# Kernel tuning notes

Hardware: AMD Instinct MI355X
Metric: run time of the kernel (lower is better)

The kernel has to match this reference:

```python
import jax, jax.numpy as jnp
import numpy as np

N_NODES = 50000
N_EDGES = 1600000
D_IN = 64
D_EDGE = 64
DIMS = [128, 128, 128]  # atom_embedding_sizes
N_GRAPHS = 64


def setup_inputs() -> dict:
    key = jax.random.key(0)
    ks = jax.random.split(key, 4 + 4 * len(DIMS))
    inp = {
        "x": jax.random.normal(ks[0], (N_NODES, D_IN), dtype=jnp.float32),
        "edge_index": jax.random.randint(ks[1], (2, N_EDGES), 0, N_NODES),
        "edge_attr": jax.random.uniform(ks[2], (N_EDGES, D_EDGE), dtype=jnp.float32),
        "batch": jnp.sort(jax.random.randint(ks[3], (N_NODES,), 0, N_GRAPHS)),
    }
    in_dim = D_IN
    ki = 4
    for l, out_dim in enumerate(DIMS):
        se = 1.0 / np.sqrt(in_dim + D_EDGE)
        sr = 1.0 / np.sqrt(in_dim)
        inp[f"We{l}"] = jax.random.uniform(ks[ki + 0], (in_dim + D_EDGE, out_dim), jnp.float32, -se, se)
        inp[f"be{l}"] = jnp.zeros((out_dim,), jnp.float32)
        inp[f"Wr{l}"] = jax.random.uniform(ks[ki + 1], (in_dim, out_dim), jnp.float32, -sr, sr)
        inp[f"br{l}"] = jnp.zeros((out_dim,), jnp.float32)
        ki += 2
        in_dim = out_dim
    return inp


def reference(x, edge_index, edge_attr, batch,
              We0, be0, Wr0, br0,
              We1, be1, Wr1, br1,
              We2, be2, Wr2, br2):
    params = [(We0, be0, Wr0, br0), (We1, be1, Wr1, br1), (We2, be2, Wr2, br2)]
    src, dst = edge_index[0], edge_index[1]  # PyG convention: messages flow src -> dst
    for We, be, Wr, br in params:
        # ESAGEConv: message = Linear([x_j || edge_attr]); add-aggregate to dst;
        # root transform Linear(x_i); then ReLU (module activation).
        msg = jnp.concatenate([x[src], edge_attr], axis=-1) @ We + be  # [E, out]
        aggr = jax.ops.segment_sum(msg, dst, num_segments=N_NODES)     # [N, out]
        x = jax.nn.relu(aggr + x @ Wr + br)
    # readout_pooling='add' -> global_add_pool over graph ids
    return jax.ops.segment_sum(x, batch, num_segments=N_GRAPHS)  # [G, out]
```

## Files before the change

### kernel.cpp

```cpp
#include <hip/hip_runtime.h>
#include <hip/hip_bf16.h>
#include <cstdint>

typedef __attribute__((ext_vector_type(8))) short short8v;
typedef __attribute__((ext_vector_type(4))) short short4v;
typedef __attribute__((ext_vector_type(4))) float f32x4;

__device__ __forceinline__ float4 add4(float4 a, float4 b) {
  return make_float4(a.x + b.x, a.y + b.y, a.z + b.z, a.w + b.w);
}
__device__ __forceinline__ float bf2f(unsigned short u) {
  union { unsigned int i; float f; } v; v.i = ((unsigned int)u) << 16; return v.f;
}
__device__ __forceinline__ unsigned short f2bf(float f) {
  union { float f; unsigned int i; } v; v.f = f;
  unsigned int r = v.i + 0x7fff + ((v.i >> 16) & 1);
  return (unsigned short)(r >> 16);
}
__device__ __forceinline__ float4 shflx4(float4 a, int m) {
  return make_float4(__shfl_xor(a.x, m, 64), __shfl_xor(a.y, m, 64),
                     __shfl_xor(a.z, m, 64), __shfl_xor(a.w, m, 64));
}
__device__ __forceinline__ void acc8(float4& lo, float4& hi, short8v v) {
  lo.x += bf2f((unsigned short)v[0]); lo.y += bf2f((unsigned short)v[1]);
  lo.z += bf2f((unsigned short)v[2]); lo.w += bf2f((unsigned short)v[3]);
  hi.x += bf2f((unsigned short)v[4]); hi.y += bf2f((unsigned short)v[5]);
  hi.z += bf2f((unsigned short)v[6]); hi.w += bf2f((unsigned short)v[7]);
}


__global__ void count_deg_kernel(const int* __restrict__ dst, int* __restrict__ deg, int E) {
  int i = blockIdx.x * blockDim.x + threadIdx.x;
  if (i < E) atomicAdd(&deg[dst[i]], 1);
}

__global__ void block_sum_kernel(const int* __restrict__ deg, int* __restrict__ bsum, int N) {
  int t = threadIdx.x;
  int i = blockIdx.x * 512 + t;
  int v = (i < N) ? deg[i] : 0;
#pragma unroll
  for (int off = 32; off > 0; off >>= 1) v += __shfl_down(v, off, 64);
  __shared__ int ws[8];
  int lane = t & 63, wid = t >> 6;
  if (lane == 0) ws[wid] = v;
  __syncthreads();
  if (t == 0) {
    int s = 0;
#pragma unroll
    for (int j = 0; j < 8; ++j) s += ws[j];
    bsum[blockIdx.x] = s;
  }
}

__global__ void scan_small_kernel(const int* __restrict__ bsum, int* __restrict__ boffs, int B) {
  int t = threadIdx.x;
  int lane = t & 63, wid = t >> 6;
  int v = (t < B) ? bsum[t] : 0;
  int incl = v;
#pragma unroll
  for (int off = 1; off < 64; off <<= 1) {
    int u = __shfl_up(incl, off, 64);
    if (lane >= off) incl += u;
  }
  __shared__ int ws[2];
  if (lane == 63) ws[wid] = incl;
  __syncthreads();
  int base = (wid == 1) ? ws[0] : 0;
  if (t < B) boffs[t] = base + incl - v;
}

__global__ void ptrs_kernel(const int* __restrict__ deg, const int* __restrict__ boffs,
                            int* __restrict__ ptrs, int N) {
  int t = threadIdx.x;
  int i = blockIdx.x * 512 + t;
  int lane = t & 63, wid = t >> 6;
  int v = (i < N) ? deg[i] : 0;
  int incl = v;
#pragma unroll
  for (int off = 1; off < 64; off <<= 1) {
    int u = __shfl_up(incl, off, 64);
    if (lane >= off) incl += u;
  }
  __shared__ int ws[8];
  if (lane == 63) ws[wid] = incl;
  __syncthreads();
  if (t == 0) {
    int s = 0;
#pragma unroll
    for (int j = 0; j < 8; ++j) { int tmp = ws[j]; ws[j] = s; s += tmp; }
  }
  __syncthreads();
  if (i < N) ptrs[i + 1] = boffs[blockIdx.x] + ws[wid] + incl;
  if (i == 0 && blockIdx.x == 0) ptrs[0] = 0;
}

__global__ void fill_csr_kernel(const int* __restrict__ src, const int* __restrict__ dst,
                                const int* __restrict__ ptrs, int* __restrict__ cnt,
                                int2* __restrict__ csr, int E) {
  int i = blockIdx.x * blockDim.x + threadIdx.x;
  if (i < E) {
    int d = dst[i];
    int pos = ptrs[d] + atomicAdd(&cnt[d], 1);
    csr[pos] = make_int2(src[i], i);
  }
}


__global__ void f2bf_stream_kernel(const float* __restrict__ in, unsigned short* __restrict__ out, int n) {
  int i = (blockIdx.x * blockDim.x + threadIdx.x) * 8;
  if (i < n) {
    float4 v0 = *(const float4*)(in + i);
    float4 v1 = *(const float4*)(in + i + 4);
    short8v o;
    o[0] = (short)f2bf(v0.x); o[1] = (short)f2bf(v0.y);
    o[2] = (short)f2bf(v0.z); o[3] = (short)f2bf(v0.w);
    o[4] = (short)f2bf(v1.x); o[5] = (short)f2bf(v1.y);
    o[6] = (short)f2bf(v1.z); o[7] = (short)f2bf(v1.w);
    *(short8v*)(out + i) = o;
  }
}

__global__ void pack_all_kernel(const float* __restrict__ We0, const float* __restrict__ Wr0,
                                const float* __restrict__ We1, const float* __restrict__ Wr1,
                                const float* __restrict__ We2, const float* __restrict__ Wr2,
                                unsigned short* __restrict__ Wt0, unsigned short* __restrict__ Wt1,
                                unsigned short* __restrict__ Wt2) {
  int idx = blockIdx.x * blockDim.x + threadIdx.x;
  const float* We; const float* Wr; unsigned short* Wt;
  int rowsE, Ktot, local;
  if (idx < 128 * 192) {
    We = We0; Wr = Wr0; Wt = Wt0; rowsE = 128; Ktot = 192; local = idx;
  } else if (idx < 128 * 192 + 128 * 320) {
    We = We1; Wr = Wr1; Wt = Wt1; rowsE = 192; Ktot = 320; local = idx - 128 * 192;
  } else if (idx < 128 * 192 + 2 * 128 * 320) {
    We = We2; Wr = Wr2; Wt = Wt2; rowsE = 192; Ktot = 320; local = idx - 128 * 192 - 128 * 320;
  } else {
    return;
  }
  int c = local / Ktot, k = local % Ktot;
  float v = (k < rowsE) ? We[(size_t)k * 128 + c] : Wr[(size_t)(k - rowsE) * 128 + c];
  Wt[local] = f2bf(v);
}

__global__ __launch_bounds__(256) void agg0_kernel(
    const int* __restrict__ ptrs, const int2* __restrict__ csr,
    const float* __restrict__ ea, const unsigned short* __restrict__ xb,
    unsigned short* __restrict__ agge, unsigned short* __restrict__ aggx64, int N) {
  int t = threadIdx.x;
  int n = blockIdx.x * 4 + (t >> 6);
  if (n >= N) return;
  int lane = t & 63;
  int slot_a = lane >> 4, cg_a = lane & 15;
  int slot_b = lane >> 3, cg_b = lane & 7;
  int s = ptrs[n], e = ptrs[n + 1];
  float4 z = make_float4(0, 0, 0, 0);
  float4 a0 = z, a1 = z;
  float4 xlo = z, xhi = z;
  int i = s;
  for (; i + 8 <= e; i += 8) {
    int e0 = csr[i + slot_a].y;
    int e1 = csr[i + 4 + slot_a].y;
    int r0 = csr[i + slot_b].x;
    a0 = add4(a0, *((const float4*)(ea + (size_t)e0 * 64) + cg_a));
    a1 = add4(a1, *((const float4*)(ea + (size_t)e1 * 64) + cg_a));
    acc8(xlo, xhi, *(const short8v*)(xb + (size_t)r0 * 64 + cg_b * 8));
  }
  if (i + slot_a < e)
    a0 = add4(a0, *((const float4*)(ea + (size_t)csr[i + slot_a].y * 64) + cg_a));
  if (i + 4 + slot_a < e)
    a1 = add4(a1, *((const float4*)(ea + (size_t)csr[i + 4 + slot_a].y * 64) + cg_a));
  if (i + slot_b < e)
    acc8(xlo, xhi, *(const short8v*)(xb + (size_t)csr[i + slot_b].x * 64 + cg_b * 8));

  a0 = add4(a0, a1);
  a0 = add4(a0, shflx4(a0, 16));
  a0 = add4(a0, shflx4(a0, 32));
  if (slot_a == 0) {
    short4v o;
    o[0] = (short)f2bf(a0.x); o[1] = (short)f2bf(a0.y);
    o[2] = (short)f2bf(a0.z); o[3] = (short)f2bf(a0.w);
    *(short4v*)(agge + (size_t)n * 64 + cg_a * 4) = o;
  }
  xlo = add4(xlo, shflx4(xlo, 8));  xhi = add4(xhi, shflx4(xhi, 8));
  xlo = add4(xlo, shflx4(xlo, 16)); xhi = add4(xhi, shflx4(xhi, 16));
  xlo = add4(xlo, shflx4(xlo, 32)); xhi = add4(xhi, shflx4(xhi, 32));
  if (slot_b == 0) {
    short8v o;
    o[0] = (short)f2bf(xlo.x); o[1] = (short)f2bf(xlo.y);
    o[2] = (short)f2bf(xlo.z); o[3] = (short)f2bf(xlo.w);
    o[4] = (short)f2bf(xhi.x); o[5] = (short)f2bf(xhi.y);
    o[6] = (short)f2bf(xhi.z); o[7] = (short)f2bf(xhi.w);
    *(short8v*)(aggx64 + (size_t)n * 64 + cg_b * 8) = o;
  }
}

__global__ __launch_bounds__(256) void agg_bf128_kernel(
    const int* __restrict__ ptrs, const int2* __restrict__ csr,
    const unsigned short* __restrict__ xb, unsigned short* __restrict__ outagg, int N) {
  int t = threadIdx.x;
  int n = blockIdx.x * 4 + (t >> 6);
  if (n >= N) return;
  int lane = t & 63;
  int slot = lane >> 4, cg = lane & 15;
  int s = ptrs[n], e = ptrs[n + 1];
  float4 lo0 = make_float4(0, 0, 0, 0), hi0 = make_float4(0, 0, 0, 0);
  float4 lo1 = make_float4(0, 0, 0, 0), hi1 = make_float4(0, 0, 0, 0);
  int i = s + slot;
  for (; i + 4 < e; i += 8) {
    acc8(lo0, hi0, *(const short8v*)(xb + (size_t)csr[i].x * 128 + cg * 8));
    acc8(lo1, hi1, *(const short8v*)(xb + (size_t)csr[i + 4].x * 128 + cg * 8));
  }
  if (i < e) acc8(lo0, hi0, *(const short8v*)(xb + (size_t)csr[i].x * 128 + cg * 8));
  lo0 = add4(lo0, lo1); hi0 = add4(hi0, hi1);
  lo0 = add4(lo0, shflx4(lo0, 16)); hi0 = add4(hi0, shflx4(hi0, 16));
  lo0 = add4(lo0, shflx4(lo0, 32)); hi0 = add4(hi0, shflx4(hi0, 32));
  if (slot == 0) {
    short8v o;
    o[0] = (short)f2bf(lo0.x); o[1] = (short)f2bf(lo0.y);
    o[2] = (short)f2bf(lo0.z); o[3] = (short)f2bf(lo0.w);
    o[4] = (short)f2bf(hi0.x); o[5] = (short)f2bf(hi0.y);
    o[6] = (short)f2bf(hi0.z); o[7] = (short)f2bf(hi0.w);
    *(short8v*)(outagg + (size_t)n * 128 + cg * 8) = o;
  }
}

template <int POOL>
__global__ __launch_bounds__(256) void gemm_mfma_kernel(
    const unsigned short* __restrict__ A1, int w1, int k1,
    const unsigned short* __restrict__ A2, int w2, int k2,
    const unsigned short* __restrict__ A3, int w3, int k3,
    const unsigned short* __restrict__ Wt, int Ktot,
    const float* __restrict__ be, const float* __restrict__ br,
    const int* __restrict__ deg, const int* __restrict__ batch,
    unsigned short* __restrict__ out, float* __restrict__ pout, int N) {
  int t = threadIdx.x;
  int wave = t >> 6, lane = t & 63;
  int rit = lane & 15, kgrp = lane >> 4;
  int n0 = blockIdx.x * 64;
  int arow = n0 + wave * 16 + rit;
  if (arow >= N) arow = N - 1;
  f32x4 acc[8];
#pragma unroll
  for (int c = 0; c < 8; ++c) acc[c] = (f32x4){0.f, 0.f, 0.f, 0.f};

  const unsigned short* As[3] = {A1, A2, A3};
  const int wds[3] = {w1, w2, w3};
  const int ks[3] = {k1, k2, k3};
  int kbase = 0;
  for (int s = 0; s < 3; ++s) {
    const unsigned short* Arow = As[s] + (size_t)arow * wds[s] + kgrp * 8;
    int K = ks[s];
    for (int kk = 0; kk < K; kk += 32) {
      short8v a = *(const short8v*)(Arow + kk);
      int kg = kbase + kk + kgrp * 8;
#pragma unroll
      for (int c = 0; c < 8; ++c) {
        short8v b = *(const short8v*)(Wt + (size_t)(c * 16 + rit) * Ktot + kg);
        acc[c] = __builtin_amdgcn_mfma_f32_16x16x32_bf16(a, b, acc[c], 0, 0, 0);
      }
    }
    kbase += K;
  }

  __shared__ unsigned short st[64][136];
  __shared__ int bsh[64];
  float dg[4];
#pragma unroll
  for (int r = 0; r < 4; ++r) {
    int n = n0 + wave * 16 + kgrp * 4 + r;
    dg[r] = (float)deg[n < N ? n : N - 1];
  }
#pragma unroll
  for (int c = 0; c < 8; ++c) {
    int col = c * 16 + rit;
    float bev = be[col], brv = br[col];
#pragma unroll
    for (int r = 0; r < 4; ++r) {
      float v = acc[c][r] + dg[r] * bev + brv;
      st[wave * 16 + kgrp * 4 + r][col] = f2bf(fmaxf(v, 0.f));
    }
  }
  if (POOL && t < 64) {
    int n = n0 + t;
    bsh[t] = (n < N) ? batch[n] : -1;
  }
  __syncthreads();

  if (POOL) {
    if (t < 128) {
      int c = t;
      float acc2 = 0.f;
      int g = bsh[0];
      for (int r = 0; r < 64; ++r) {
        int n = n0 + r;
        if (n >= N) break;
        int gn = bsh[r];
        if (gn != g) {
          atomicAdd(&pout[g * 128 + c], acc2);
          acc2 = 0.f;
          g = gn;
        }
        acc2 += bf2f(st[r][c]);
      }
      atomicAdd(&pout[g * 128 + c], acc2);
    }
  } else {
#pragma unroll
    for (int it = 0; it < 4; ++it) {
      int idx = t + it * 256;
      int row = idx >> 4, cg = idx & 15;
      int n = n0 + row;
      if (n < N)
        *(short8v*)(out + (size_t)n * 128 + cg * 8) = *(const short8v*)(&st[row][cg * 8]);
    }
  }
}


extern "C" void kernel_launch(void* const* d_in, const int* in_sizes, int n_in,
                              void* d_out, int out_size, void* d_ws, size_t ws_size,
                              hipStream_t stream) {
  const float* x_in       = (const float*)d_in[0];
  const int*   edge_index = (const int*)d_in[1];
  const float* edge_attr  = (const float*)d_in[2];
  const int*   batch      = (const int*)d_in[3];
  const float* We0 = (const float*)d_in[4];
  const float* be0 = (const float*)d_in[5];
  const float* Wr0 = (const float*)d_in[6];
  const float* br0 = (const float*)d_in[7];
  const float* We1 = (const float*)d_in[8];
  const float* be1 = (const float*)d_in[9];
  const float* Wr1 = (const float*)d_in[10];
  const float* br1 = (const float*)d_in[11];
  const float* We2 = (const float*)d_in[12];
  const float* be2 = (const float*)d_in[13];
  const float* Wr2 = (const float*)d_in[14];
  const float* br2 = (const float*)d_in[15];

  float* out = (float*)d_out;

  int N = in_sizes[0] / 64;
  int E = in_sizes[1] / 2;
  const int* src = edge_index;
  const int* dst = edge_index + E;

  char* w = (char*)d_ws;
  size_t off = 0;
  auto alloc = [&](size_t bytes) {
    void* p = w + off;
    off += (bytes + 255) & ~(size_t)255;
    return p;
  };
  int* deg   = (int*)alloc((size_t)N * 4);
  int* cnt   = (int*)alloc((size_t)N * 4);
  size_t zero_bytes = off;
  int* ptrs  = (int*)alloc((size_t)(N + 1) * 4);
  int* bsum  = (int*)alloc(128 * 4);
  int* boffs = (int*)alloc(128 * 4);
  int2* csr  = (int2*)alloc((size_t)E * 8);
  unsigned short* x_bf   = (unsigned short*)alloc((size_t)N * 64 * 2);
  unsigned short* aggx64 = (unsigned short*)alloc((size_t)N * 64 * 2);
  unsigned short* agge   = (unsigned short*)alloc((size_t)N * 64 * 2);
  unsigned short* aggx   = (unsigned short*)alloc((size_t)N * 128 * 2);
  unsigned short* xb0    = (unsigned short*)alloc((size_t)N * 128 * 2);
  unsigned short* xb1    = (unsigned short*)alloc((size_t)N * 128 * 2);
  unsigned short* Wt0    = (unsigned short*)alloc((size_t)128 * 192 * 2);
  unsigned short* Wt1    = (unsigned short*)alloc((size_t)128 * 320 * 2);
  unsigned short* Wt2    = (unsigned short*)alloc((size_t)128 * 320 * 2);

  (void)hipMemsetAsync(d_ws, 0, zero_bytes, stream);
  (void)hipMemsetAsync(d_out, 0, (size_t)out_size * sizeof(float), stream);

  int eb = (E + 255) / 256;
  int sb = (N + 511) / 512;
  count_deg_kernel<<<eb, 256, 0, stream>>>(dst, deg, E);
  block_sum_kernel<<<sb, 512, 0, stream>>>(deg, bsum, N);
  scan_small_kernel<<<1, 128, 0, stream>>>(bsum, boffs, sb);
  ptrs_kernel<<<sb, 512, 0, stream>>>(deg, boffs, ptrs, N);
  fill_csr_kernel<<<eb, 256, 0, stream>>>(src, dst, ptrs, cnt, csr, E);

  f2bf_stream_kernel<<<(N * 64 / 8 + 255) / 256, 256, 0, stream>>>(x_in, x_bf, N * 64);
  {
    int total = 128 * 192 + 2 * 128 * 320;
    pack_all_kernel<<<(total + 255) / 256, 256, 0, stream>>>(We0, Wr0, We1, Wr1, We2, Wr2,
                                                             Wt0, Wt1, Wt2);
  }

  int gb = (N + 63) / 64;
  int ab = (N + 3) / 4;

  agg0_kernel<<<ab, 256, 0, stream>>>(ptrs, csr, edge_attr, x_bf, agge, aggx64, N);

  gemm_mfma_kernel<0><<<gb, 256, 0, stream>>>(aggx64, 64, 64, agge, 64, 64, x_bf, 64, 64,
                                              Wt0, 192, be0, br0, deg, batch, xb0, nullptr, N);
  agg_bf128_kernel<<<ab, 256, 0, stream>>>(ptrs, csr, xb0, aggx, N);
  gemm_mfma_kernel<0><<<gb, 256, 0, stream>>>(aggx, 128, 128, agge, 64, 64, xb0, 128, 128,
                                              Wt1, 320, be1, br1, deg, batch, xb1, nullptr, N);
  agg_bf128_kernel<<<ab, 256, 0, stream>>>(ptrs, csr, xb1, aggx, N);
  gemm_mfma_kernel<1><<<gb, 256, 0, stream>>>(aggx, 128, 128, agge, 64, 64, xb1, 128, 128,
                                              Wt2, 320, be2, br2, deg, batch, nullptr, out, N);
}
```

Measured before the change: 491.1 us.

## Fuse per-layer aggregation into MFMA GEMM via shared memory, merge prep kernels

Each layer's neighbour aggregation now writes its result straight into a shared-memory tile that the MFMA GEMM in the same 1024-thread block reads, so the aggregated activations no longer round-trip through global memory. Degree counting, x-to-bf16 conversion and weight packing are merged into one grid-stride prep kernel, cutting launch count. The CSR is split from an int2 array into separate src and edge-id arrays, so later layers only stream the src indices. In exchange the fused kernel runs aggregation and GEMM phases back to back without overlap, and the large blocks with shared tiles may limit occupancy.

```diff
diff --git a/kernel.cpp b/kernel.cpp
--- a/kernel.cpp
+++ b/kernel.cpp
@@ -28,10 +28,38 @@
   hi.z += bf2f((unsigned short)v[6]); hi.w += bf2f((unsigned short)v[7]);
 }
 
-
-__global__ void count_deg_kernel(const int* __restrict__ dst, int* __restrict__ deg, int E) {
-  int i = blockIdx.x * blockDim.x + threadIdx.x;
-  if (i < E) atomicAdd(&deg[dst[i]], 1);
+__global__ __launch_bounds__(256) void prep_kernel(
+    const int* __restrict__ dst, int* __restrict__ deg, int E,
+    const float* __restrict__ x_in, unsigned short* __restrict__ x_bf, int nx8,
+    const float* __restrict__ We0, const float* __restrict__ Wr0,
+    const float* __restrict__ We1, const float* __restrict__ Wr1,
+    const float* __restrict__ We2, const float* __restrict__ Wr2,
+    unsigned short* __restrict__ Wt0, unsigned short* __restrict__ Wt1,
+    unsigned short* __restrict__ Wt2) {
+  int gs = gridDim.x * 256;
+  int gid = blockIdx.x * 256 + threadIdx.x;
+  for (int i = gid; i < E; i += gs) atomicAdd(&deg[dst[i]], 1);
+  for (int i = gid; i < nx8; i += gs) {
+    float4 v0 = *(const float4*)(x_in + i * 8);
+    float4 v1 = *(const float4*)(x_in + i * 8 + 4);
+    short8v o;
+    o[0] = (short)f2bf(v0.x); o[1] = (short)f2bf(v0.y);
+    o[2] = (short)f2bf(v0.z); o[3] = (short)f2bf(v0.w);
+    o[4] = (short)f2bf(v1.x); o[5] = (short)f2bf(v1.y);
+    o[6] = (short)f2bf(v1.z); o[7] = (short)f2bf(v1.w);
+    *(short8v*)(x_bf + i * 8) = o;
+  }
+  const int p0 = 128 * 192, p1 = 128 * 320;
+  for (int idx = gid; idx < p0 + 2 * p1; idx += gs) {
+    const float* We; const float* Wr; unsigned short* Wt;
+    int rowsE, Ktot, local;
+    if (idx < p0) { We = We0; Wr = Wr0; Wt = Wt0; rowsE = 128; Ktot = 192; local = idx; }
+    else if (idx < p0 + p1) { We = We1; Wr = Wr1; Wt = Wt1; rowsE = 192; Ktot = 320; local = idx - p0; }
+    else { We = We2; Wr = Wr2; Wt = Wt2; rowsE = 192; Ktot = 320; local = idx - p0 - p1; }
+    int c = local / Ktot, k = local % Ktot;
+    float v = (k < rowsE) ? We[(size_t)k * 128 + c] : Wr[(size_t)(k - rowsE) * 128 + c];
+    Wt[local] = f2bf(v);
+  }
 }
 
 __global__ void block_sum_kernel(const int* __restrict__ deg, int* __restrict__ bsum, int N) {
@@ -96,193 +124,161 @@
 
 __global__ void fill_csr_kernel(const int* __restrict__ src, const int* __restrict__ dst,
                                 const int* __restrict__ ptrs, int* __restrict__ cnt,
-                                int2* __restrict__ csr, int E) {
+                                int* __restrict__ csr_src, int* __restrict__ csr_eid, int E) {
   int i = blockIdx.x * blockDim.x + threadIdx.x;
   if (i < E) {
     int d = dst[i];
     int pos = ptrs[d] + atomicAdd(&cnt[d], 1);
-    csr[pos] = make_int2(src[i], i);
-  }
-}
-
-
-__global__ void f2bf_stream_kernel(const float* __restrict__ in, unsigned short* __restrict__ out, int n) {
-  int i = (blockIdx.x * blockDim.x + threadIdx.x) * 8;
-  if (i < n) {
-    float4 v0 = *(const float4*)(in + i);
-    float4 v1 = *(const float4*)(in + i + 4);
-    short8v o;
-    o[0] = (short)f2bf(v0.x); o[1] = (short)f2bf(v0.y);
-    o[2] = (short)f2bf(v0.z); o[3] = (short)f2bf(v0.w);
-    o[4] = (short)f2bf(v1.x); o[5] = (short)f2bf(v1.y);
-    o[6] = (short)f2bf(v1.z); o[7] = (short)f2bf(v1.w);
-    *(short8v*)(out + i) = o;
-  }
-}
-
-__global__ void pack_all_kernel(const float* __restrict__ We0, const float* __restrict__ Wr0,
-                                const float* __restrict__ We1, const float* __restrict__ Wr1,
-                                const float* __restrict__ We2, const float* __restrict__ Wr2,
-                                unsigned short* __restrict__ Wt0, unsigned short* __restrict__ Wt1,
-                                unsigned short* __restrict__ Wt2) {
-  int idx = blockIdx.x * blockDim.x + threadIdx.x;
-  const float* We; const float* Wr; unsigned short* Wt;
-  int rowsE, Ktot, local;
-  if (idx < 128 * 192) {
-    We = We0; Wr = Wr0; Wt = Wt0; rowsE = 128; Ktot = 192; local = idx;
-  } else if (idx < 128 * 192 + 128 * 320) {
-    We = We1; Wr = Wr1; Wt = Wt1; rowsE = 192; Ktot = 320; local = idx - 128 * 192;
-  } else if (idx < 128 * 192 + 2 * 128 * 320) {
-    We = We2; Wr = Wr2; Wt = Wt2; rowsE = 192; Ktot = 320; local = idx - 128 * 192 - 128 * 320;
-  } else {
-    return;
-  }
-  int c = local / Ktot, k = local % Ktot;
-  float v = (k < rowsE) ? We[(size_t)k * 128 + c] : Wr[(size_t)(k - rowsE) * 128 + c];
-  Wt[local] = f2bf(v);
-}
-
-__global__ __launch_bounds__(256) void agg0_kernel(
-    const int* __restrict__ ptrs, const int2* __restrict__ csr,
-    const float* __restrict__ ea, const unsigned short* __restrict__ xb,
-    unsigned short* __restrict__ agge, unsigned short* __restrict__ aggx64, int N) {
-  int t = threadIdx.x;
-  int n = blockIdx.x * 4 + (t >> 6);
-  if (n >= N) return;
-  int lane = t & 63;
-  int slot_a = lane >> 4, cg_a = lane & 15;
-  int slot_b = lane >> 3, cg_b = lane & 7;
-  int s = ptrs[n], e = ptrs[n + 1];
-  float4 z = make_float4(0, 0, 0, 0);
-  float4 a0 = z, a1 = z;
-  float4 xlo = z, xhi = z;
-  int i = s;
-  for (; i + 8 <= e; i += 8) {
-    int e0 = csr[i + slot_a].y;
-    int e1 = csr[i + 4 + slot_a].y;
-    int r0 = csr[i + slot_b].x;
-    a0 = add4(a0, *((const float4*)(ea + (size_t)e0 * 64) + cg_a));
-    a1 = add4(a1, *((const float4*)(ea + (size_t)e1 * 64) + cg_a));
-    acc8(xlo, xhi, *(const short8v*)(xb + (size_t)r0 * 64 + cg_b * 8));
-  }
-  if (i + slot_a < e)
-    a0 = add4(a0, *((const float4*)(ea + (size_t)csr[i + slot_a].y * 64) + cg_a));
-  if (i + 4 + slot_a < e)
-    a1 = add4(a1, *((const float4*)(ea + (size_t)csr[i + 4 + slot_a].y * 64) + cg_a));
-  if (i + slot_b < e)
-    acc8(xlo, xhi, *(const short8v*)(xb + (size_t)csr[i + slot_b].x * 64 + cg_b * 8));
-
-  a0 = add4(a0, a1);
-  a0 = add4(a0, shflx4(a0, 16));
-  a0 = add4(a0, shflx4(a0, 32));
-  if (slot_a == 0) {
-    short4v o;
-    o[0] = (short)f2bf(a0.x); o[1] = (short)f2bf(a0.y);
-    o[2] = (short)f2bf(a0.z); o[3] = (short)f2bf(a0.w);
-    *(short4v*)(agge + (size_t)n * 64 + cg_a * 4) = o;
-  }
-  xlo = add4(xlo, shflx4(xlo, 8));  xhi = add4(xhi, shflx4(xhi, 8));
-  xlo = add4(xlo, shflx4(xlo, 16)); xhi = add4(xhi, shflx4(xhi, 16));
-  xlo = add4(xlo, shflx4(xlo, 32)); xhi = add4(xhi, shflx4(xhi, 32));
-  if (slot_b == 0) {
-    short8v o;
-    o[0] = (short)f2bf(xlo.x); o[1] = (short)f2bf(xlo.y);
-    o[2] = (short)f2bf(xlo.z); o[3] = (short)f2bf(xlo.w);
-    o[4] = (short)f2bf(xhi.x); o[5] = (short)f2bf(xhi.y);
-    o[6] = (short)f2bf(xhi.z); o[7] = (short)f2bf(xhi.w);
-    *(short8v*)(aggx64 + (size_t)n * 64 + cg_b * 8) = o;
-  }
-}
-
-__global__ __launch_bounds__(256) void agg_bf128_kernel(
-    const int* __restrict__ ptrs, const int2* __restrict__ csr,
-    const unsigned short* __restrict__ xb, unsigned short* __restrict__ outagg, int N) {
-  int t = threadIdx.x;
-  int n = blockIdx.x * 4 + (t >> 6);
-  if (n >= N) return;
-  int lane = t & 63;
-  int slot = lane >> 4, cg = lane & 15;
-  int s = ptrs[n], e = ptrs[n + 1];
-  float4 lo0 = make_float4(0, 0, 0, 0), hi0 = make_float4(0, 0, 0, 0);
-  float4 lo1 = make_float4(0, 0, 0, 0), hi1 = make_float4(0, 0, 0, 0);
-  int i = s + slot;
-  for (; i + 4 < e; i += 8) {
-    acc8(lo0, hi0, *(const short8v*)(xb + (size_t)csr[i].x * 128 + cg * 8));
-    acc8(lo1, hi1, *(const short8v*)(xb + (size_t)csr[i + 4].x * 128 + cg * 8));
-  }
-  if (i < e) acc8(lo0, hi0, *(const short8v*)(xb + (size_t)csr[i].x * 128 + cg * 8));
-  lo0 = add4(lo0, lo1); hi0 = add4(hi0, hi1);
-  lo0 = add4(lo0, shflx4(lo0, 16)); hi0 = add4(hi0, shflx4(hi0, 16));
-  lo0 = add4(lo0, shflx4(lo0, 32)); hi0 = add4(hi0, shflx4(hi0, 32));
-  if (slot == 0) {
-    short8v o;
-    o[0] = (short)f2bf(lo0.x); o[1] = (short)f2bf(lo0.y);
-    o[2] = (short)f2bf(lo0.z); o[3] = (short)f2bf(lo0.w);
-    o[4] = (short)f2bf(hi0.x); o[5] = (short)f2bf(hi0.y);
-    o[6] = (short)f2bf(hi0.z); o[7] = (short)f2bf(hi0.w);
-    *(short8v*)(outagg + (size_t)n * 128 + cg * 8) = o;
-  }
-}
-
-template <int POOL>
-__global__ __launch_bounds__(256) void gemm_mfma_kernel(
-    const unsigned short* __restrict__ A1, int w1, int k1,
-    const unsigned short* __restrict__ A2, int w2, int k2,
-    const unsigned short* __restrict__ A3, int w3, int k3,
+    csr_src[pos] = src[i];
+    csr_eid[pos] = i;
+  }
+}
+
+template <int L0, int POOL>
+__global__ __launch_bounds__(1024, 8) void fused_layer_kernel(
+    const int* __restrict__ ptrs, const int* __restrict__ csr_src, const int* __restrict__ csr_eid,
+    const float* __restrict__ ea, const unsigned short* __restrict__ xprev,
+    const unsigned short* __restrict__ agge_r, unsigned short* __restrict__ agge_w,
     const unsigned short* __restrict__ Wt, int Ktot,
     const float* __restrict__ be, const float* __restrict__ br,
     const int* __restrict__ deg, const int* __restrict__ batch,
     unsigned short* __restrict__ out, float* __restrict__ pout, int N) {
   int t = threadIdx.x;
-  int wave = t >> 6, lane = t & 63;
-  int rit = lane & 15, kgrp = lane >> 4;
+  int wv = t >> 6, lane = t & 63;
   int n0 = blockIdx.x * 64;
-  int arow = n0 + wave * 16 + rit;
-  if (arow >= N) arow = N - 1;
-  f32x4 acc[8];
-#pragma unroll
-  for (int c = 0; c < 8; ++c) acc[c] = (f32x4){0.f, 0.f, 0.f, 0.f};
-
-  const unsigned short* As[3] = {A1, A2, A3};
-  const int wds[3] = {w1, w2, w3};
-  const int ks[3] = {k1, k2, k3};
-  int kbase = 0;
-  for (int s = 0; s < 3; ++s) {
-    const unsigned short* Arow = As[s] + (size_t)arow * wds[s] + kgrp * 8;
-    int K = ks[s];
-    for (int kk = 0; kk < K; kk += 32) {
-      short8v a = *(const short8v*)(Arow + kk);
-      int kg = kbase + kk + kgrp * 8;
-#pragma unroll
-      for (int c = 0; c < 8; ++c) {
-        short8v b = *(const short8v*)(Wt + (size_t)(c * 16 + rit) * Ktot + kg);
-        acc[c] = __builtin_amdgcn_mfma_f32_16x16x32_bf16(a, b, acc[c], 0, 0, 0);
-      }
-    }
-    kbase += K;
-  }
-
+  __shared__ unsigned short sA[64][136];
   __shared__ unsigned short st[64][136];
   __shared__ int bsh[64];
-  float dg[4];
-#pragma unroll
-  for (int r = 0; r < 4; ++r) {
-    int n = n0 + wave * 16 + kgrp * 4 + r;
-    dg[r] = (float)deg[n < N ? n : N - 1];
-  }
-#pragma unroll
-  for (int c = 0; c < 8; ++c) {
-    int col = c * 16 + rit;
-    float bev = be[col], brv = br[col];
-#pragma unroll
-    for (int r = 0; r < 4; ++r) {
-      float v = acc[c][r] + dg[r] * bev + brv;
-      st[wave * 16 + kgrp * 4 + r][col] = f2bf(fmaxf(v, 0.f));
+
+  const int xw = L0 ? 64 : 128;
+
+  for (int j = 0; j < 4; ++j) {
+    int lr = wv * 4 + j;
+    int n = n0 + lr;
+    int s = 0, e = 0;
+    if (n < N) { s = ptrs[n]; e = ptrs[n + 1]; }
+    if (L0) {
+      int slot_a = lane >> 4, cg_a = lane & 15;
+      int slot_b = lane >> 3, cg_b = lane & 7;
+      float4 z = make_float4(0, 0, 0, 0);
+      float4 a0 = z, a1 = z, xlo = z, xhi = z;
+      int i = s;
+      for (; i + 8 <= e; i += 8) {
+        int e0 = csr_eid[i + slot_a];
+        int e1 = csr_eid[i + 4 + slot_a];
+        int r0 = csr_src[i + slot_b];
+        a0 = add4(a0, *((const float4*)(ea + (size_t)e0 * 64) + cg_a));
+        a1 = add4(a1, *((const float4*)(ea + (size_t)e1 * 64) + cg_a));
+        acc8(xlo, xhi, *(const short8v*)(xprev + (size_t)r0 * 64 + cg_b * 8));
+      }
+      if (i + slot_a < e)
+        a0 = add4(a0, *((const float4*)(ea + (size_t)csr_eid[i + slot_a] * 64) + cg_a));
+      if (i + 4 + slot_a < e)
+        a1 = add4(a1, *((const float4*)(ea + (size_t)csr_eid[i + 4 + slot_a] * 64) + cg_a));
+      if (i + slot_b < e)
+        acc8(xlo, xhi, *(const short8v*)(xprev + (size_t)csr_src[i + slot_b] * 64 + cg_b * 8));
+      a0 = add4(a0, a1);
+      a0 = add4(a0, shflx4(a0, 16));
+      a0 = add4(a0, shflx4(a0, 32));
+      if (slot_a == 0) {
+        short4v o;
+        o[0] = (short)f2bf(a0.x); o[1] = (short)f2bf(a0.y);
+        o[2] = (short)f2bf(a0.z); o[3] = (short)f2bf(a0.w);
+        *(short4v*)(&sA[lr][64 + cg_a * 4]) = o;
+        if (n < N) *(short4v*)(agge_w + (size_t)n * 64 + cg_a * 4) = o;
+      }
+      xlo = add4(xlo, shflx4(xlo, 8));  xhi = add4(xhi, shflx4(xhi, 8));
+      xlo = add4(xlo, shflx4(xlo, 16)); xhi = add4(xhi, shflx4(xhi, 16));
+      xlo = add4(xlo, shflx4(xlo, 32)); xhi = add4(xhi, shflx4(xhi, 32));
+      if (slot_b == 0) {
+        short8v o;
+        o[0] = (short)f2bf(xlo.x); o[1] = (short)f2bf(xlo.y);
+        o[2] = (short)f2bf(xlo.z); o[3] = (short)f2bf(xlo.w);
+        o[4] = (short)f2bf(xhi.x); o[5] = (short)f2bf(xhi.y);
+        o[6] = (short)f2bf(xhi.z); o[7] = (short)f2bf(xhi.w);
+        *(short8v*)(&sA[lr][cg_b * 8]) = o;
+      }
+    } else {
+      int slot = lane >> 4, cg = lane & 15;
+      float4 z = make_float4(0, 0, 0, 0);
+      float4 lo0 = z, hi0 = z, lo1 = z, hi1 = z;
+      int i = s + slot;
+      for (; i + 4 < e; i += 8) {
+        acc8(lo0, hi0, *(const short8v*)(xprev + (size_t)csr_src[i] * 128 + cg * 8));
+        acc8(lo1, hi1, *(const short8v*)(xprev + (size_t)csr_src[i + 4] * 128 + cg * 8));
+      }
+      if (i < e) acc8(lo0, hi0, *(const short8v*)(xprev + (size_t)csr_src[i] * 128 + cg * 8));
+      lo0 = add4(lo0, lo1); hi0 = add4(hi0, hi1);
+      lo0 = add4(lo0, shflx4(lo0, 16)); hi0 = add4(hi0, shflx4(hi0, 16));
+      lo0 = add4(lo0, shflx4(lo0, 32)); hi0 = add4(hi0, shflx4(hi0, 32));
+      if (slot == 0) {
+        short8v o;
+        o[0] = (short)f2bf(lo0.x); o[1] = (short)f2bf(lo0.y);
+        o[2] = (short)f2bf(lo0.z); o[3] = (short)f2bf(lo0.w);
+        o[4] = (short)f2bf(hi0.x); o[5] = (short)f2bf(hi0.y);
+        o[6] = (short)f2bf(hi0.z); o[7] = (short)f2bf(hi0.w);
+        *(short8v*)(&sA[lr][cg * 8]) = o;
+      }
     }
   }
   if (POOL && t < 64) {
     int n = n0 + t;
     bsh[t] = (n < N) ? batch[n] : -1;
+  }
+  __syncthreads();
+
+  int rit = lane & 15, kgrp = lane >> 4;
+  int rt = wv & 3, cp = wv >> 2;
+  int arow_l = rt * 16 + rit;
+  int arow_g = n0 + arow_l;
+  if (arow_g >= N) arow_g = N - 1;
+  f32x4 acc0 = (f32x4){0.f, 0.f, 0.f, 0.f};
+  f32x4 acc1 = (f32x4){0.f, 0.f, 0.f, 0.f};
+  const unsigned short* WtA = Wt + (size_t)((cp * 2 + 0) * 16 + rit) * Ktot;
+  const unsigned short* WtB = Wt + (size_t)((cp * 2 + 1) * 16 + rit) * Ktot;
+
+#pragma unroll
+  for (int kk = 0; kk < 128; kk += 32) {
+    int kg = kk + kgrp * 8;
+    short8v a = *(const short8v*)(&sA[arow_l][kg]);
+    acc0 = __builtin_amdgcn_mfma_f32_16x16x32_bf16(a, *(const short8v*)(WtA + kg), acc0, 0, 0, 0);
+    acc1 = __builtin_amdgcn_mfma_f32_16x16x32_bf16(a, *(const short8v*)(WtB + kg), acc1, 0, 0, 0);
+  }
+  int kbase = 128;
+  if (!L0) {
+#pragma unroll
+    for (int kk = 0; kk < 64; kk += 32) {
+      int kg = kbase + kk + kgrp * 8;
+      short8v a = *(const short8v*)(agge_r + (size_t)arow_g * 64 + kk + kgrp * 8);
+      acc0 = __builtin_amdgcn_mfma_f32_16x16x32_bf16(a, *(const short8v*)(WtA + kg), acc0, 0, 0, 0);
+      acc1 = __builtin_amdgcn_mfma_f32_16x16x32_bf16(a, *(const short8v*)(WtB + kg), acc1, 0, 0, 0);
+    }
+    kbase += 64;
+  }
+#pragma unroll
+  for (int kk = 0; kk < (L0 ? 64 : 128); kk += 32) {
+    int kg = kbase + kk + kgrp * 8;
+    short8v a = *(const short8v*)(xprev + (size_t)arow_g * xw + kk + kgrp * 8);
+    acc0 = __builtin_amdgcn_mfma_f32_16x16x32_bf16(a, *(const short8v*)(WtA + kg), acc0, 0, 0, 0);
+    acc1 = __builtin_amdgcn_mfma_f32_16x16x32_bf16(a, *(const short8v*)(WtB + kg), acc1, 0, 0, 0);
+  }
+
+  float dg[4];
+#pragma unroll
+  for (int r = 0; r < 4; ++r) {
+    int n = n0 + rt * 16 + kgrp * 4 + r;
+    dg[r] = (float)deg[n < N ? n : N - 1];
+  }
+#pragma unroll
+  for (int c = 0; c < 2; ++c) {
+    int col = (cp * 2 + c) * 16 + rit;
+    float bev = be[col], brv = br[col];
+    f32x4 a = c ? acc1 : acc0;
+#pragma unroll
+    for (int r = 0; r < 4; ++r) {
+      float v = a[r] + dg[r] * bev + brv;
+      st[rt * 16 + kgrp * 4 + r][col] = f2bf(fmaxf(v, 0.f));
+    }
   }
   __syncthreads();
 
@@ -305,14 +301,10 @@
       atomicAdd(&pout[g * 128 + c], acc2);
     }
   } else {
-#pragma unroll
-    for (int it = 0; it < 4; ++it) {
-      int idx = t + it * 256;
-      int row = idx >> 4, cg = idx & 15;
-      int n = n0 + row;
-      if (n < N)
-        *(short8v*)(out + (size_t)n * 128 + cg * 8) = *(const short8v*)(&st[row][cg * 8]);
-    }
+    int row = t >> 4, cg = t & 15;
+    int n = n0 + row;
+    if (n < N)
+      *(short8v*)(out + (size_t)n * 128 + cg * 8) = *(const short8v*)(&st[row][cg * 8]);
   }
 }
 
@@ -351,52 +343,42 @@
     off += (bytes + 255) & ~(size_t)255;
     return p;
   };
-  int* deg   = (int*)alloc((size_t)N * 4);
-  int* cnt   = (int*)alloc((size_t)N * 4);
+  int* deg     = (int*)alloc((size_t)N * 4);
+  int* cnt     = (int*)alloc((size_t)N * 4);
   size_t zero_bytes = off;
-  int* ptrs  = (int*)alloc((size_t)(N + 1) * 4);
-  int* bsum  = (int*)alloc(128 * 4);
-  int* boffs = (int*)alloc(128 * 4);
-  int2* csr  = (int2*)alloc((size_t)E * 8);
-  unsigned short* x_bf   = (unsigned short*)alloc((size_t)N * 64 * 2);
-  unsigned short* aggx64 = (unsigned short*)alloc((size_t)N * 64 * 2);
-  unsigned short* agge   = (unsigned short*)alloc((size_t)N * 64 * 2);
-  unsigned short* aggx   = (unsigned short*)alloc((size_t)N * 128 * 2);
-  unsigned short* xb0    = (unsigned short*)alloc((size_t)N * 128 * 2);
-  unsigned short* xb1    = (unsigned short*)alloc((size_t)N * 128 * 2);
-  unsigned short* Wt0    = (unsigned short*)alloc((size_t)128 * 192 * 2);
-  unsigned short* Wt1    = (unsigned short*)alloc((size_t)128 * 320 * 2);
-  unsigned short* Wt2    = (unsigned short*)alloc((size_t)128 * 320 * 2);
+  int* ptrs    = (int*)alloc((size_t)(N + 1) * 4);
+  int* bsum    = (int*)alloc(128 * 4);
+  int* boffs   = (int*)alloc(128 * 4);
+  int* csr_src = (int*)alloc((size_t)E * 4);
+  int* csr_eid = (int*)alloc((size_t)E * 4);
+  unsigned short* x_bf = (unsigned short*)alloc((size_t)N * 64 * 2);
+  unsigned short* agge = (unsigned short*)alloc((size_t)N * 64 * 2);
+  unsigned short* xb0  = (unsigned short*)alloc((size_t)N * 128 * 2);
+  unsigned short* xb1  = (unsigned short*)alloc((size_t)N * 128 * 2);
+  unsigned short* Wt0  = (unsigned short*)alloc((size_t)128 * 192 * 2);
+  unsigned short* Wt1  = (unsigned short*)alloc((size_t)128 * 320 * 2);
+  unsigned short* Wt2  = (unsigned short*)alloc((size_t)128 * 320 * 2);
 
   (void)hipMemsetAsync(d_ws, 0, zero_bytes, stream);
   (void)hipMemsetAsync(d_out, 0, (size_t)out_size * sizeof(float), stream);
 
   int eb = (E + 255) / 256;
   int sb = (N + 511) / 512;
-  count_deg_kernel<<<eb, 256, 0, stream>>>(dst, deg, E);
+  prep_kernel<<<2048, 256, 0, stream>>>(dst, deg, E, x_in, x_bf, N * 64 / 8,
+                                        We0, Wr0, We1, Wr1, We2, Wr2, Wt0, Wt1, Wt2);
   block_sum_kernel<<<sb, 512, 0, stream>>>(deg, bsum, N);
   scan_small_kernel<<<1, 128, 0, stream>>>(bsum, boffs, sb);
   ptrs_kernel<<<sb, 512, 0, stream>>>(deg, boffs, ptrs, N);
-  fill_csr_kernel<<<eb, 256, 0, stream>>>(src, dst, ptrs, cnt, csr, E);
-
-  f2bf_stream_kernel<<<(N * 64 / 8 + 255) / 256, 256, 0, stream>>>(x_in, x_bf, N * 64);
-  {
-    int total = 128 * 192 + 2 * 128 * 320;
-    pack_all_kernel<<<(total + 255) / 256, 256, 0, stream>>>(We0, Wr0, We1, Wr1, We2, Wr2,
-                                                             Wt0, Wt1, Wt2);
-  }
+  fill_csr_kernel<<<eb, 256, 0, stream>>>(src, dst, ptrs, cnt, csr_src, csr_eid, E);
 
   int gb = (N + 63) / 64;
-  int ab = (N + 3) / 4;
-
-  agg0_kernel<<<ab, 256, 0, stream>>>(ptrs, csr, edge_attr, x_bf, agge, aggx64, N);
-
-  gemm_mfma_kernel<0><<<gb, 256, 0, stream>>>(aggx64, 64, 64, agge, 64, 64, x_bf, 64, 64,
-                                              Wt0, 192, be0, br0, deg, batch, xb0, nullptr, N);
-  agg_bf128_kernel<<<ab, 256, 0, stream>>>(ptrs, csr, xb0, aggx, N);
-  gemm_mfma_kernel<0><<<gb, 256, 0, stream>>>(aggx, 128, 128, agge, 64, 64, xb0, 128, 128,
-                                              Wt1, 320, be1, br1, deg, batch, xb1, nullptr, N);
-  agg_bf128_kernel<<<ab, 256, 0, stream>>>(ptrs, csr, xb1, aggx, N);
-  gemm_mfma_kernel<1><<<gb, 256, 0, stream>>>(aggx, 128, 128, agge, 64, 64, xb1, 128, 128,
-                                              Wt2, 320, be2, br2, deg, batch, nullptr, out, N);
-}
+  fused_layer_kernel<1, 0><<<gb, 1024, 0, stream>>>(ptrs, csr_src, csr_eid, edge_attr, x_bf,
+                                                    nullptr, agge, Wt0, 192, be0, br0,
+                                                    deg, batch, xb0, nullptr, N);
+  fused_layer_kernel<0, 0><<<gb, 1024, 0, stream>>>(ptrs, csr_src, nullptr, nullptr, xb0,
+                                                    agge, nullptr, Wt1, 320, be1, br1,
+                                                    deg, batch, xb1, nullptr, N);
+  fused_layer_kernel<0, 1><<<gb, 1024, 0, stream>>>(ptrs, csr_src, nullptr, nullptr, xb1,
+                                                    agge, nullptr, Wt2, 320, be2, br2,
+                                                    deg, batch, nullptr, out, N);
+}
```

Result: slower. 521.5 us (+6.2%).

## Split CSR into separate src/eid arrays and fuse prep kernels

Applied to the files above, without the earlier changes.

Replaces the interleaved int2 CSR array with two separate int arrays, so the layer-1/2 aggregation kernels read only source indices and move half as many index bytes. It also merges the degree count, x-to-bf16 conversion and weight packing into one grid-stride prep kernel, which removes two launches. The trade-off is that fill_csr now issues two scattered stores per edge instead of one.

```diff
diff --git a/kernel.cpp b/kernel.cpp
--- a/kernel.cpp
+++ b/kernel.cpp
@@ -28,122 +28,114 @@
   hi.z += bf2f((unsigned short)v[6]); hi.w += bf2f((unsigned short)v[7]);
 }
 
-
-__global__ void count_deg_kernel(const int* __restrict__ dst, int* __restrict__ deg, int E) {
-  int i = blockIdx.x * blockDim.x + threadIdx.x;
-  if (i < E) atomicAdd(&deg[dst[i]], 1);
-}
-
-__global__ void block_sum_kernel(const int* __restrict__ deg, int* __restrict__ bsum, int N) {
-  int t = threadIdx.x;
-  int i = blockIdx.x * 512 + t;
-  int v = (i < N) ? deg[i] : 0;
-#pragma unroll
-  for (int off = 32; off > 0; off >>= 1) v += __shfl_down(v, off, 64);
-  __shared__ int ws[8];
-  int lane = t & 63, wid = t >> 6;
-  if (lane == 0) ws[wid] = v;
-  __syncthreads();
-  if (t == 0) {
-    int s = 0;
-#pragma unroll
-    for (int j = 0; j < 8; ++j) s += ws[j];
-    bsum[blockIdx.x] = s;
-  }
-}
-
-__global__ void scan_small_kernel(const int* __restrict__ bsum, int* __restrict__ boffs, int B) {
-  int t = threadIdx.x;
-  int lane = t & 63, wid = t >> 6;
-  int v = (t < B) ? bsum[t] : 0;
-  int incl = v;
-#pragma unroll
-  for (int off = 1; off < 64; off <<= 1) {
-    int u = __shfl_up(incl, off, 64);
-    if (lane >= off) incl += u;
-  }
-  __shared__ int ws[2];
-  if (lane == 63) ws[wid] = incl;
-  __syncthreads();
-  int base = (wid == 1) ? ws[0] : 0;
-  if (t < B) boffs[t] = base + incl - v;
-}
-
-__global__ void ptrs_kernel(const int* __restrict__ deg, const int* __restrict__ boffs,
-                            int* __restrict__ ptrs, int N) {
-  int t = threadIdx.x;
-  int i = blockIdx.x * 512 + t;
-  int lane = t & 63, wid = t >> 6;
-  int v = (i < N) ? deg[i] : 0;
-  int incl = v;
-#pragma unroll
-  for (int off = 1; off < 64; off <<= 1) {
-    int u = __shfl_up(incl, off, 64);
-    if (lane >= off) incl += u;
-  }
-  __shared__ int ws[8];
-  if (lane == 63) ws[wid] = incl;
-  __syncthreads();
-  if (t == 0) {
-    int s = 0;
-#pragma unroll
-    for (int j = 0; j < 8; ++j) { int tmp = ws[j]; ws[j] = s; s += tmp; }
-  }
-  __syncthreads();
-  if (i < N) ptrs[i + 1] = boffs[blockIdx.x] + ws[wid] + incl;
-  if (i == 0 && blockIdx.x == 0) ptrs[0] = 0;
-}
-
-__global__ void fill_csr_kernel(const int* __restrict__ src, const int* __restrict__ dst,
-                                const int* __restrict__ ptrs, int* __restrict__ cnt,
-                                int2* __restrict__ csr, int E) {
-  int i = blockIdx.x * blockDim.x + threadIdx.x;
-  if (i < E) {
-    int d = dst[i];
-    int pos = ptrs[d] + atomicAdd(&cnt[d], 1);
-    csr[pos] = make_int2(src[i], i);
-  }
-}
-
-
-__global__ void f2bf_stream_kernel(const float* __restrict__ in, unsigned short* __restrict__ out, int n) {
-  int i = (blockIdx.x * blockDim.x + threadIdx.x) * 8;
-  if (i < n) {
-    float4 v0 = *(const float4*)(in + i);
-    float4 v1 = *(const float4*)(in + i + 4);
+__global__ __launch_bounds__(256) void prep_kernel(
+    const int* __restrict__ dst, int* __restrict__ deg, int E,
+    const float* __restrict__ x_in, unsigned short* __restrict__ x_bf, int nx8,
+    const float* __restrict__ We0, const float* __restrict__ Wr0,
+    const float* __restrict__ We1, const float* __restrict__ Wr1,
+    const float* __restrict__ We2, const float* __restrict__ Wr2,
+    unsigned short* __restrict__ Wt0, unsigned short* __restrict__ Wt1,
+    unsigned short* __restrict__ Wt2) {
+  int gs = gridDim.x * 256;
+  int gid = blockIdx.x * 256 + threadIdx.x;
+  for (int i = gid; i < E; i += gs) atomicAdd(&deg[dst[i]], 1);
+  for (int i = gid; i < nx8; i += gs) {
+    float4 v0 = *(const float4*)(x_in + i * 8);
+    float4 v1 = *(const float4*)(x_in + i * 8 + 4);
     short8v o;
     o[0] = (short)f2bf(v0.x); o[1] = (short)f2bf(v0.y);
     o[2] = (short)f2bf(v0.z); o[3] = (short)f2bf(v0.w);
     o[4] = (short)f2bf(v1.x); o[5] = (short)f2bf(v1.y);
     o[6] = (short)f2bf(v1.z); o[7] = (short)f2bf(v1.w);
-    *(short8v*)(out + i) = o;
-  }
-}
-
-__global__ void pack_all_kernel(const float* __restrict__ We0, const float* __restrict__ Wr0,
-                                const float* __restrict__ We1, const float* __restrict__ Wr1,
-                                const float* __restrict__ We2, const float* __restrict__ Wr2,
-                                unsigned short* __restrict__ Wt0, unsigned short* __restrict__ Wt1,
-                                unsigned short* __restrict__ Wt2) {
-  int idx = blockIdx.x * blockDim.x + threadIdx.x;
-  const float* We; const float* Wr; unsigned short* Wt;
-  int rowsE, Ktot, local;
-  if (idx < 128 * 192) {
-    We = We0; Wr = Wr0; Wt = Wt0; rowsE = 128; Ktot = 192; local = idx;
-  } else if (idx < 128 * 192 + 128 * 320) {
-    We = We1; Wr = Wr1; Wt = Wt1; rowsE = 192; Ktot = 320; local = idx - 128 * 192;
-  } else if (idx < 128 * 192 + 2 * 128 * 320) {
-    We = We2; Wr = Wr2; Wt = Wt2; rowsE = 192; Ktot = 320; local = idx - 128 * 192 - 128 * 320;
-  } else {
-    return;
-  }
-  int c = local / Ktot, k = local % Ktot;
-  float v = (k < rowsE) ? We[(size_t)k * 128 + c] : Wr[(size_t)(k - rowsE) * 128 + c];
-  Wt[local] = f2bf(v);
+    *(short8v*)(x_bf + i * 8) = o;
+  }
+  const int p0 = 128 * 192, p1 = 128 * 320;
+  for (int idx = gid; idx < p0 + 2 * p1; idx += gs) {
+    const float* We; const float* Wr; unsigned short* Wt;
+    int rowsE, Ktot, local;
+    if (idx < p0) { We = We0; Wr = Wr0; Wt = Wt0; rowsE = 128; Ktot = 192; local = idx; }
+    else if (idx < p0 + p1) { We = We1; Wr = Wr1; Wt = Wt1; rowsE = 192; Ktot = 320; local = idx - p0; }
+    else { We = We2; Wr = Wr2; Wt = Wt2; rowsE = 192; Ktot = 320; local = idx - p0 - p1; }
+    int c = local / Ktot, k = local % Ktot;
+    float v = (k < rowsE) ? We[(size_t)k * 128 + c] : Wr[(size_t)(k - rowsE) * 128 + c];
+    Wt[local] = f2bf(v);
+  }
+}
+
+__global__ void block_sum_kernel(const int* __restrict__ deg, int* __restrict__ bsum, int N) {
+  int t = threadIdx.x;
+  int i = blockIdx.x * 512 + t;
+  int v = (i < N) ? deg[i] : 0;
+#pragma unroll
+  for (int off = 32; off > 0; off >>= 1) v += __shfl_down(v, off, 64);
+  __shared__ int ws[8];
+  int lane = t & 63, wid = t >> 6;
+  if (lane == 0) ws[wid] = v;
+  __syncthreads();
+  if (t == 0) {
+    int s = 0;
+#pragma unroll
+    for (int j = 0; j < 8; ++j) s += ws[j];
+    bsum[blockIdx.x] = s;
+  }
+}
+
+__global__ void scan_small_kernel(const int* __restrict__ bsum, int* __restrict__ boffs, int B) {
+  int t = threadIdx.x;
+  int lane = t & 63, wid = t >> 6;
+  int v = (t < B) ? bsum[t] : 0;
+  int incl = v;
+#pragma unroll
+  for (int off = 1; off < 64; off <<= 1) {
+    int u = __shfl_up(incl, off, 64);
+    if (lane >= off) incl += u;
+  }
+  __shared__ int ws[2];
+  if (lane == 63) ws[wid] = incl;
+  __syncthreads();
+  int base = (wid == 1) ? ws[0] : 0;
+  if (t < B) boffs[t] = base + incl - v;
+}
+
+__global__ void ptrs_kernel(const int* __restrict__ deg, const int* __restrict__ boffs,
+                            int* __restrict__ ptrs, int N) {
+  int t = threadIdx.x;
+  int i = blockIdx.x * 512 + t;
+  int lane = t & 63, wid = t >> 6;
+  int v = (i < N) ? deg[i] : 0;
+  int incl = v;
+#pragma unroll
+  for (int off = 1; off < 64; off <<= 1) {
+    int u = __shfl_up(incl, off, 64);
+    if (lane >= off) incl += u;
+  }
+  __shared__ int ws[8];
+  if (lane == 63) ws[wid] = incl;
+  __syncthreads();
+  if (t == 0) {
+    int s = 0;
+#pragma unroll
+    for (int j = 0; j < 8; ++j) { int tmp = ws[j]; ws[j] = s; s += tmp; }
+  }
+  __syncthreads();
+  if (i < N) ptrs[i + 1] = boffs[blockIdx.x] + ws[wid] + incl;
+  if (i == 0 && blockIdx.x == 0) ptrs[0] = 0;
+}
+
+__global__ void fill_csr_kernel(const int* __restrict__ src, const int* __restrict__ dst,
+                                const int* __restrict__ ptrs, int* __restrict__ cnt,
+                                int* __restrict__ csr_src, int* __restrict__ csr_eid, int E) {
+  int i = blockIdx.x * blockDim.x + threadIdx.x;
+  if (i < E) {
+    int d = dst[i];
+    int pos = ptrs[d] + atomicAdd(&cnt[d], 1);
+    csr_src[pos] = src[i];
+    csr_eid[pos] = i;
+  }
 }
 
 __global__ __launch_bounds__(256) void agg0_kernel(
-    const int* __restrict__ ptrs, const int2* __restrict__ csr,
+    const int* __restrict__ ptrs, const int* __restrict__ csr_src, const int* __restrict__ csr_eid,
     const float* __restrict__ ea, const unsigned short* __restrict__ xb,
     unsigned short* __restrict__ agge, unsigned short* __restrict__ aggx64, int N) {
   int t = threadIdx.x;
@@ -158,19 +150,19 @@
   float4 xlo = z, xhi = z;
   int i = s;
   for (; i + 8 <= e; i += 8) {
-    int e0 = csr[i + slot_a].y;
-    int e1 = csr[i + 4 + slot_a].y;
-    int r0 = csr[i + slot_b].x;
+    int e0 = csr_eid[i + slot_a];
+    int e1 = csr_eid[i + 4 + slot_a];
+    int r0 = csr_src[i + slot_b];
     a0 = add4(a0, *((const float4*)(ea + (size_t)e0 * 64) + cg_a));
     a1 = add4(a1, *((const float4*)(ea + (size_t)e1 * 64) + cg_a));
     acc8(xlo, xhi, *(const short8v*)(xb + (size_t)r0 * 64 + cg_b * 8));
   }
   if (i + slot_a < e)
-    a0 = add4(a0, *((const float4*)(ea + (size_t)csr[i + slot_a].y * 64) + cg_a));
+    a0 = add4(a0, *((const float4*)(ea + (size_t)csr_eid[i + slot_a] * 64) + cg_a));
   if (i + 4 + slot_a < e)
-    a1 = add4(a1, *((const float4*)(ea + (size_t)csr[i + 4 + slot_a].y * 64) + cg_a));
+    a1 = add4(a1, *((const float4*)(ea + (size_t)csr_eid[i + 4 + slot_a] * 64) + cg_a));
   if (i + slot_b < e)
-    acc8(xlo, xhi, *(const short8v*)(xb + (size_t)csr[i + slot_b].x * 64 + cg_b * 8));
+    acc8(xlo, xhi, *(const short8v*)(xb + (size_t)csr_src[i + slot_b] * 64 + cg_b * 8));
 
   a0 = add4(a0, a1);
   a0 = add4(a0, shflx4(a0, 16));
@@ -195,7 +187,7 @@
 }
 
 __global__ __launch_bounds__(256) void agg_bf128_kernel(
-    const int* __restrict__ ptrs, const int2* __restrict__ csr,
+    const int* __restrict__ ptrs, const int* __restrict__ csr_src,
     const unsigned short* __restrict__ xb, unsigned short* __restrict__ outagg, int N) {
   int t = threadIdx.x;
   int n = blockIdx.x * 4 + (t >> 6);
@@ -207,10 +199,10 @@
   float4 lo1 = make_float4(0, 0, 0, 0), hi1 = make_float4(0, 0, 0, 0);
   int i = s + slot;
   for (; i + 4 < e; i += 8) {
-    acc8(lo0, hi0, *(const short8v*)(xb + (size_t)csr[i].x * 128 + cg * 8));
-    acc8(lo1, hi1, *(const short8v*)(xb + (size_t)csr[i + 4].x * 128 + cg * 8));
-  }
-  if (i < e) acc8(lo0, hi0, *(const short8v*)(xb + (size_t)csr[i].x * 128 + cg * 8));
+    acc8(lo0, hi0, *(const short8v*)(xb + (size_t)csr_src[i] * 128 + cg * 8));
+    acc8(lo1, hi1, *(const short8v*)(xb + (size_t)csr_src[i + 4] * 128 + cg * 8));
+  }
+  if (i < e) acc8(lo0, hi0, *(const short8v*)(xb + (size_t)csr_src[i] * 128 + cg * 8));
   lo0 = add4(lo0, lo1); hi0 = add4(hi0, hi1);
   lo0 = add4(lo0, shflx4(lo0, 16)); hi0 = add4(hi0, shflx4(hi0, 16));
   lo0 = add4(lo0, shflx4(lo0, 32)); hi0 = add4(hi0, shflx4(hi0, 32));
@@ -351,13 +343,14 @@
     off += (bytes + 255) & ~(size_t)255;
     return p;
   };
-  int* deg   = (int*)alloc((size_t)N * 4);
-  int* cnt   = (int*)alloc((size_t)N * 4);
+  int* deg     = (int*)alloc((size_t)N * 4);
+  int* cnt     = (int*)alloc((size_t)N * 4);
   size_t zero_bytes = off;
-  int* ptrs  = (int*)alloc((size_t)(N + 1) * 4);
-  int* bsum  = (int*)alloc(128 * 4);
-  int* boffs = (int*)alloc(128 * 4);
-  int2* csr  = (int2*)alloc((size_t)E * 8);
+  int* ptrs    = (int*)alloc((size_t)(N + 1) * 4);
+  int* bsum    = (int*)alloc(128 * 4);
+  int* boffs   = (int*)alloc(128 * 4);
+  int* csr_src = (int*)alloc((size_t)E * 4);
+  int* csr_eid = (int*)alloc((size_t)E * 4);
   unsigned short* x_bf   = (unsigned short*)alloc((size_t)N * 64 * 2);
   unsigned short* aggx64 = (unsigned short*)alloc((size_t)N * 64 * 2);
   unsigned short* agge   = (unsigned short*)alloc((size_t)N * 64 * 2);
@@ -373,30 +366,24 @@
 
   int eb = (E + 255) / 256;
   int sb = (N + 511) / 512;
-  count_deg_kernel<<<eb, 256, 0, stream>>>(dst, deg, E);
+  prep_kernel<<<2048, 256, 0, stream>>>(dst, deg, E, x_in, x_bf, N * 64 / 8,
+                                        We0, Wr0, We1, Wr1, We2, Wr2, Wt0, Wt1, Wt2);
   block_sum_kernel<<<sb, 512, 0, stream>>>(deg, bsum, N);
   scan_small_kernel<<<1, 128, 0, stream>>>(bsum, boffs, sb);
   ptrs_kernel<<<sb, 512, 0, stream>>>(deg, boffs, ptrs, N);
-  fill_csr_kernel<<<eb, 256, 0, stream>>>(src, dst, ptrs, cnt, csr, E);
-
-  f2bf_stream_kernel<<<(N * 64 / 8 + 255) / 256, 256, 0, stream>>>(x_in, x_bf, N * 64);
-  {
-    int total = 128 * 192 + 2 * 128 * 320;
-    pack_all_kernel<<<(total + 255) / 256, 256, 0, stream>>>(We0, Wr0, We1, Wr1, We2, Wr2,
-                                                             Wt0, Wt1, Wt2);
-  }
+  fill_csr_kernel<<<eb, 256, 0, stream>>>(src, dst, ptrs, cnt, csr_src, csr_eid, E);
 
   int gb = (N + 63) / 64;
   int ab = (N + 3) / 4;
 
-  agg0_kernel<<<ab, 256, 0, stream>>>(ptrs, csr, edge_attr, x_bf, agge, aggx64, N);
+  agg0_kernel<<<ab, 256, 0, stream>>>(ptrs, csr_src, csr_eid, edge_attr, x_bf, agge, aggx64, N);
 
   gemm_mfma_kernel<0><<<gb, 256, 0, stream>>>(aggx64, 64, 64, agge, 64, 64, x_bf, 64, 64,
                                               Wt0, 192, be0, br0, deg, batch, xb0, nullptr, N);
-  agg_bf128_kernel<<<ab, 256, 0, stream>>>(ptrs, csr, xb0, aggx, N);
+  agg_bf128_kernel<<<ab, 256, 0, stream>>>(ptrs, csr_src, xb0, aggx, N);
   gemm_mfma_kernel<0><<<gb, 256, 0, stream>>>(aggx, 128, 128, agge, 64, 64, xb0, 128, 128,
                                               Wt1, 320, be1, br1, deg, batch, xb1, nullptr, N);
-  agg_bf128_kernel<<<ab, 256, 0, stream>>>(ptrs, csr, xb1, aggx, N);
+  agg_bf128_kernel<<<ab, 256, 0, stream>>>(ptrs, csr_src, xb1, aggx, N);
   gemm_mfma_kernel<1><<<gb, 256, 0, stream>>>(aggx, 128, 128, agge, 64, 64, xb1, 128, 128,
                                               Wt2, 320, be2, br2, deg, batch, nullptr, out, N);
 }
```

New measurement: 496.7 us (median of 2 runs). Within noise of the previous version (+1.1%).
